# Kernel tuning notes

Hardware: AMD Instinct MI355X
Metric: run time of the kernel (lower is better)

Reference implementation:

```python
import jax, jax.numpy as jnp
import numpy as np

EMB = 256  # embedding_dim


def setup_inputs() -> dict:
    key = jax.random.key(0)
    ks = jax.random.split(key, 9)
    B, S, D = 4, 4096, EMB
    inputs = jax.random.normal(ks[0], (B, S, 3 * D), dtype=jnp.float32)
    def dense(kw, kb, d_in, d_out):
        w = jax.random.normal(kw, (d_in, d_out), dtype=jnp.float32) / np.sqrt(d_in)
        b = jnp.zeros((d_out,), dtype=jnp.float32)
        return w, b
    wq, bq = dense(ks[1], ks[2], D, D)
    wk, bk = dense(ks[3], ks[4], D, D)
    wv, bv = dense(ks[5], ks[6], D, D)
    wo, bo = dense(ks[7], ks[8], D, D)
    return {"inputs": inputs, "wq": wq, "bq": bq, "wk": wk, "bk": bk,
            "wv": wv, "bv": bv, "wo": wo, "bo": bo}


def reference(inputs, wq, bq, wk, bk, wv, bv, wo, bo):
    # split last axis into q,k,v parts: [B,S,D] each
    q_in, k_in, v_in = jnp.split(inputs, 3, axis=-1)
    q = q_in @ wq + bq
    k = k_in @ wk + bk
    v = v_in @ wv + bv
    dk = jnp.asarray(k.shape[-1], dtype=jnp.float32)
    # unfused SDPA exactly as source: matmul -> scale -> softmax -> matmul
    logits = jnp.einsum('bsd,btd->bst', q, k) / jnp.sqrt(dk)  # [B,S,S]
    attn = jax.nn.softmax(logits, axis=-1)
    x = jnp.einsum('bst,btd->bsd', attn, v)
    return x @ wo + bo
```

## Files before the change

### kernel.cpp

```cpp
#include <hip/hip_runtime.h>

typedef _Float16 f16;
typedef _Float16 f16x4 __attribute__((ext_vector_type(4)));
typedef _Float16 f16x8 __attribute__((ext_vector_type(8)));
typedef float f32x4  __attribute__((ext_vector_type(4)));

#define MFMAH(a, b, c) __builtin_amdgcn_mfma_f32_16x16x32_f16(a, b, c, 0, 0, 0)

constexpr int D = 256;
constexpr int S = 4096;
constexpr int BATCH = 4;
constexpr int NROWS = BATCH * S;
constexpr float SCALE = 0.0625f;
constexpr size_t NE = (size_t)NROWS * D;

__device__ __forceinline__ void gll16(const void* g, void* l) {
  __builtin_amdgcn_global_load_lds(
      (const __attribute__((address_space(1))) unsigned int*)g,
      (__attribute__((address_space(3))) unsigned int*)l, 16, 0, 0);
}

__global__ __launch_bounds__(256)
void prep_wt_kernel(const float* __restrict__ wq, const float* __restrict__ wk,
                    const float* __restrict__ wv, const float* __restrict__ wo,
                    f16* __restrict__ Wt)
{
  const int m = blockIdx.y;
  const float* w = (m == 0) ? wq : (m == 1) ? wk : (m == 2) ? wv : wo;
  int id = blockIdx.x * 256 + threadIdx.x;
  int n = id >> 8, k = id & 255;
  Wt[((size_t)m << 16) + n * 256 + k] = (f16)w[k * 256 + n];
}

__global__ __launch_bounds__(256)
void qkv_mfma_kernel(const float* __restrict__ in, const f16* __restrict__ Wt,
                     const float* __restrict__ bq, const float* __restrict__ bk,
                     const float* __restrict__ bv,
                     f16* __restrict__ Qh, f16* __restrict__ Kf, f16* __restrict__ Vf)
{
  __shared__ __align__(16) char smem[32768];
  const int m = blockIdx.y;
  const int tid = threadIdx.x, lane = tid & 63, w = tid >> 6;
  const int l15 = lane & 15, quad = lane >> 4;
  const int row0 = blockIdx.x * 64 + w * 16;
  const f16* Wm = Wt + ((size_t)m << 16);
  const float* bias = (m == 0) ? bq : (m == 1) ? bk : bv;

  f16x8 af[8];
  {
    const float* arow = in + (size_t)(row0 + l15) * 768 + m * 256 + quad * 8;
#pragma unroll
    for (int kc = 0; kc < 8; ++kc) {
      float4 a0 = *(const float4*)(arow + kc * 32);
      float4 a1 = *(const float4*)(arow + kc * 32 + 4);
      f16x8 a;
      a[0] = (f16)a0.x; a[1] = (f16)a0.y; a[2] = (f16)a0.z; a[3] = (f16)a0.w;
      a[4] = (f16)a1.x; a[5] = (f16)a1.y; a[6] = (f16)a1.z; a[7] = (f16)a1.w;
      af[kc] = a;
    }
  }

  auto stageB = [&](int buf, int kc) {
    char* base = smem + buf * 16384;
#pragma unroll
    for (int i = 0; i < 4; ++i) {
      int ct = 4 * w + i;
      gll16(Wm + (ct * 16 + l15) * 256 + kc * 32 + quad * 8,
            base + ct * 1024 + lane * 16);
    }
  };

  f32x4 acc[16];
#pragma unroll
  for (int ct = 0; ct < 16; ++ct) acc[ct] = (f32x4){0.f, 0.f, 0.f, 0.f};

  stageB(0, 0);
  for (int kc = 0; kc < 8; ++kc) {
    __syncthreads();
    if (kc < 7) stageB((kc + 1) & 1, kc + 1);
    const char* Bb = smem + (kc & 1) * 16384;
#pragma unroll
    for (int ct = 0; ct < 16; ++ct) {
      f16x8 b = *(const f16x8*)(Bb + ct * 1024 + lane * 16);
      acc[ct] = MFMAH(af[kc], b, acc[ct]);
    }
  }
  __syncthreads();

  const int b_ = row0 >> 12;

  if (m == 0) {
    f16* ws = (f16*)(smem + w * 8192);
#pragma unroll
    for (int ct = 0; ct < 16; ++ct) {
      float bct = bias[ct * 16 + l15];
#pragma unroll
      for (int r = 0; r < 4; ++r)
        ws[(quad * 4 + r) * 256 + ct * 16 + l15] = (f16)((acc[ct][r] + bct) * SCALE);
    }
    f16* dst = Qh + (size_t)row0 * 256;
#pragma unroll
    for (int i = 0; i < 8; ++i)
      *(uint4*)(dst + lane * 8 + i * 512) = *(const uint4*)(ws + lane * 8 + i * 512);
  } else if (m == 1) {
    f16* ws = (f16*)(smem + w * 8192);
#pragma unroll
    for (int ct = 0; ct < 16; ++ct) {
      float bct = bias[ct * 16 + l15];
      int base = (ct >> 1) * 512 + ((ct & 1) * 2 + (l15 >> 3)) * 128 + (l15 & 7);
#pragma unroll
      for (int r = 0; r < 4; ++r)
        ws[base + (quad * 4 + r) * 8] = (f16)(acc[ct][r] + bct);
    }
    const int g = (row0 & 4095) >> 4;
    f16* dst = Kf + ((size_t)(b_ * 256 + g)) * 8 * 512;
#pragma unroll
    for (int i = 0; i < 8; ++i)
      *(uint4*)(dst + lane * 8 + i * 512) = *(const uint4*)(ws + lane * 8 + i * 512);
  } else {
    const int t = w & 1;
    f16* ws = (f16*)(smem + (w >> 1) * 16384);
#pragma unroll
    for (int ct = 0; ct < 16; ++ct) {
      float bct = bias[ct * 16 + l15];
      int base = ct * 512 + quad * 128 + l15 * 8 + t * 4;
#pragma unroll
      for (int r = 0; r < 4; ++r)
        ws[base + r] = (f16)(acc[ct][r] + bct);
    }
    __syncthreads();
    const int gv0 = ((blockIdx.x * 64) & 4095) >> 5;
    f16* dst = Vf + ((size_t)(b_ * 128 + gv0)) * 16 * 512;
    const f16* src = (const f16*)smem;
#pragma unroll
    for (int i = 0; i < 8; ++i)
      *(uint4*)(dst + tid * 8 + i * 2048) = *(const uint4*)(src + tid * 8 + i * 2048);
  }
}

__global__ __launch_bounds__(256, 2)
void attn6_kernel(const f16* __restrict__ Qh, const char* __restrict__ Kf,
                  const char* __restrict__ Vf,
                  f16* __restrict__ Pp, float* __restrict__ Mp, float* __restrict__ Lp)
{
  __shared__ __align__(16) char KVs[2][32768];

  const int tid = threadIdx.x, lane = tid & 63, w = tid >> 6;
  const int l15 = lane & 15, quad = lane >> 4;

  const int bx    = blockIdx.x;
  const int combo = bx & 15;
  const int b     = combo & 3;
  const int kz    = combo >> 2;
  const int qb    = bx >> 4;
  const int qrow0 = qb * 128 + w * 32;
  const int grow  = b * 4096 + qrow0;

  f16x8 qf[2][8];
#pragma unroll
  for (int sub = 0; sub < 2; ++sub) {
    const size_t qoff = (size_t)(grow + sub * 16 + l15) * 256 + quad * 8;
#pragma unroll
    for (int kc = 0; kc < 8; ++kc)
      qf[sub][kc] = *(const f16x8*)(Qh + qoff + kc * 32);
  }

  const char* kg[4];
  const char* vg[4];
#pragma unroll
  for (int i = 0; i < 4; ++i) {
    int f = 4 * w + i;
    kg[i] = Kf + (((size_t)(b * 256 + kz * 64 + (f >> 3))) * 8 + (f & 7)) * 1024
               + lane * 16;
    vg[i] = Vf + (((size_t)(b * 128 + kz * 32)) * 16 + f) * 1024 + lane * 16;
  }
  auto stage = [&](int buf) {
    char* base = &KVs[buf][0];
#pragma unroll
    for (int i = 0; i < 4; ++i) { gll16(kg[i], base + (4 * w + i) * 1024); kg[i] += 16384; }
#pragma unroll
    for (int i = 0; i < 4; ++i) { gll16(vg[i], base + 16384 + (4 * w + i) * 1024); vg[i] += 16384; }
  };

  f32x4 o0[16], o1[16];
#pragma unroll
  for (int ct = 0; ct < 16; ++ct) {
    o0[ct] = (f32x4){0.f, 0.f, 0.f, 0.f};
    o1[ct] = (f32x4){0.f, 0.f, 0.f, 0.f};
  }
  float m0 = -3.0e38f, m1 = -3.0e38f, l0 = 0.f, l1 = 0.f;

  stage(0);

  for (int it = 0; it < 32; ++it) {
    __syncthreads();
    if (it < 31) stage((it + 1) & 1);
    const char* Bf = &KVs[it & 1][0];

    f32x4 sA0 = (f32x4){0.f,0.f,0.f,0.f}, sB0 = (f32x4){0.f,0.f,0.f,0.f};
    f32x4 sA1 = (f32x4){0.f,0.f,0.f,0.f}, sB1 = (f32x4){0.f,0.f,0.f,0.f};
#pragma unroll
    for (int kc = 0; kc < 8; ++kc) {
      f16x8 kA = *(const f16x8*)(Bf + kc * 1024 + lane * 16);
      f16x8 kB = *(const f16x8*)(Bf + 8192 + kc * 1024 + lane * 16);
      sA0 = MFMAH(kA, qf[0][kc], sA0);
      sA1 = MFMAH(kA, qf[1][kc], sA1);
      sB0 = MFMAH(kB, qf[0][kc], sB0);
      sB1 = MFMAH(kB, qf[1][kc], sB1);
    }

    float mn0, mn1, al0, al1;
    f16x8 ph0, ph1;
    {
      float t = fmaxf(fmaxf(fmaxf(sA0[0], sA0[1]), fmaxf(sA0[2], sA0[3])),
                      fmaxf(fmaxf(sB0[0], sB0[1]), fmaxf(sB0[2], sB0[3])));
      t = fmaxf(t, __shfl_xor(t, 16));
      t = fmaxf(t, __shfl_xor(t, 32));
      mn0 = fmaxf(m0, t);
      al0 = __expf(m0 - mn0);
      float ps = 0.f;
#pragma unroll
      for (int r = 0; r < 4; ++r) {
        float pa = __expf(sA0[r] - mn0);
        float pb = __expf(sB0[r] - mn0);
        ph0[r] = (f16)pa;  ph0[r + 4] = (f16)pb;
        ps += pa + pb;
      }
      ps += __shfl_xor(ps, 16);
      ps += __shfl_xor(ps, 32);
      l0 = l0 * al0 + ps;
    }
    {
      float t = fmaxf(fmaxf(fmaxf(sA1[0], sA1[1]), fmaxf(sA1[2], sA1[3])),
                      fmaxf(fmaxf(sB1[0], sB1[1]), fmaxf(sB1[2], sB1[3])));
      t = fmaxf(t, __shfl_xor(t, 16));
      t = fmaxf(t, __shfl_xor(t, 32));
      mn1 = fmaxf(m1, t);
      al1 = __expf(m1 - mn1);
      float ps = 0.f;
#pragma unroll
      for (int r = 0; r < 4; ++r) {
        float pa = __expf(sA1[r] - mn1);
        float pb = __expf(sB1[r] - mn1);
        ph1[r] = (f16)pa;  ph1[r + 4] = (f16)pb;
        ps += pa + pb;
      }
      ps += __shfl_xor(ps, 16);
      ps += __shfl_xor(ps, 32);
      l1 = l1 * al1 + ps;
    }

    if (__any(mn0 > m0)) {
      float a0 = __shfl(al0, (quad << 2) + 0);
      float a1 = __shfl(al0, (quad << 2) + 1);
      float a2 = __shfl(al0, (quad << 2) + 2);
      float a3 = __shfl(al0, (quad << 2) + 3);
#pragma unroll
      for (int ct = 0; ct < 16; ++ct) {
        o0[ct][0] *= a0; o0[ct][1] *= a1; o0[ct][2] *= a2; o0[ct][3] *= a3;
      }
    }
    if (__any(mn1 > m1)) {
      float a0 = __shfl(al1, (quad << 2) + 0);
      float a1 = __shfl(al1, (quad << 2) + 1);
      float a2 = __shfl(al1, (quad << 2) + 2);
      float a3 = __shfl(al1, (quad << 2) + 3);
#pragma unroll
      for (int ct = 0; ct < 16; ++ct) {
        o1[ct][0] *= a0; o1[ct][1] *= a1; o1[ct][2] *= a2; o1[ct][3] *= a3;
      }
    }
    m0 = mn0;  m1 = mn1;

#pragma unroll
    for (int ct = 0; ct < 16; ++ct) {
      f16x8 vf = *(const f16x8*)(Bf + 16384 + ct * 1024 + lane * 16);
      o0[ct] = MFMAH(ph0, vf, o0[ct]);
      o1[ct] = MFMAH(ph1, vf, o1[ct]);
    }
  }

  f16* Od = Pp + (size_t)kz * NE;
#pragma unroll
  for (int r = 0; r < 4; ++r) {
    const size_t ro0 = (size_t)(grow + quad * 4 + r) * 256 + l15;
    const size_t ro1 = (size_t)(grow + 16 + quad * 4 + r) * 256 + l15;
#pragma unroll
    for (int ct = 0; ct < 16; ++ct) {
      Od[ro0 + ct * 16] = (f16)o0[ct][r];
      Od[ro1 + ct * 16] = (f16)o1[ct][r];
    }
  }
  if (lane < 16) {
    Mp[kz * NROWS + grow + l15] = m0;
    Lp[kz * NROWS + grow + l15] = l0;
    Mp[kz * NROWS + grow + 16 + l15] = m1;
    Lp[kz * NROWS + grow + 16 + l15] = l1;
  }
}

__global__ __launch_bounds__(256)
void oproj_mfma_kernel(const f16* __restrict__ Pp, const float* __restrict__ Mp,
                       const float* __restrict__ Lp, const f16* __restrict__ Wto,
                       const float* __restrict__ bo, float* __restrict__ out)
{
  __shared__ f16 xs[32][264];
  __shared__ __align__(16) char Bs[2][16384];
  const int tid = threadIdx.x, lane = tid & 63, w = tid >> 6;
  const int l15 = lane & 15, quad = lane >> 4;
  const int rb = blockIdx.x * 32;

  auto stageB = [&](int buf, int kc) {
    char* base = &Bs[buf][0];
#pragma unroll
    for (int i = 0; i < 4; ++i) {
      int ct = 4 * w + i;
      gll16(Wto + (ct * 16 + l15) * 256 + kc * 32 + quad * 8,
            base + ct * 1024 + lane * 16);
    }
  };
  stageB(0, 0);

  const int c4 = (tid & 63) * 4;
  const int rsub = tid >> 6;
#pragma unroll
  for (int e = 0; e < 8; ++e) {
    int rl = e * 4 + rsub;
    int row = rb + rl;
    float m[4], l[4];
#pragma unroll
    for (int z = 0; z < 4; ++z) {
      m[z] = Mp[z * NROWS + row];
      l[z] = Lp[z * NROWS + row];
    }
    float mm = fmaxf(fmaxf(m[0], m[1]), fmaxf(m[2], m[3]));
    float wz[4], denom = 0.f;
#pragma unroll
    for (int z = 0; z < 4; ++z) { wz[z] = __expf(m[z] - mm); denom += wz[z] * l[z]; }
    float inv = 1.0f / denom;
    float s0 = 0.f, s1 = 0.f, s2 = 0.f, s3 = 0.f;
#pragma unroll
    for (int z = 0; z < 4; ++z) {
      f16x4 h = *(const f16x4*)(Pp + (size_t)z * NE + (size_t)row * 256 + c4);
      s0 += wz[z] * (float)h[0];
      s1 += wz[z] * (float)h[1];
      s2 += wz[z] * (float)h[2];
      s3 += wz[z] * (float)h[3];
    }
    f16x4 xv;
    xv[0] = (f16)(s0 * inv); xv[1] = (f16)(s1 * inv);
    xv[2] = (f16)(s2 * inv); xv[3] = (f16)(s3 * inv);
    *(f16x4*)&xs[rl][c4] = xv;
  }

  const int rw = (w & 1) * 16;
  const int cg = (w >> 1) * 8;
  f32x4 acc[8];
#pragma unroll
  for (int c = 0; c < 8; ++c) acc[c] = (f32x4){0.f, 0.f, 0.f, 0.f};

  for (int kc = 0; kc < 8; ++kc) {
    __syncthreads();
    if (kc < 7) stageB((kc + 1) & 1, kc + 1);
    const char* Bb = &Bs[kc & 1][0];
    f16x8 a = *(const f16x8*)&xs[rw + l15][kc * 32 + quad * 8];
#pragma unroll
    for (int c = 0; c < 8; ++c) {
      f16x8 b = *(const f16x8*)(Bb + (cg + c) * 1024 + lane * 16);
      acc[c] = MFMAH(a, b, acc[c]);
    }
  }

#pragma unroll
  for (int c = 0; c < 8; ++c) {
    int col = (cg + c) * 16 + l15;
    float bct = bo[col];
#pragma unroll
    for (int r = 0; r < 4; ++r)
      out[(size_t)(rb + rw + quad * 4 + r) * 256 + col] = acc[c][r] + bct;
  }
}

extern "C" void kernel_launch(void* const* d_in, const int* in_sizes, int n_in,
                              void* d_out, int out_size, void* d_ws, size_t ws_size,
                              hipStream_t stream)
{
  const float* inp = (const float*)d_in[0];
  const float* wq  = (const float*)d_in[1];
  const float* bq  = (const float*)d_in[2];
  const float* wk  = (const float*)d_in[3];
  const float* bk  = (const float*)d_in[4];
  const float* wv  = (const float*)d_in[5];
  const float* bv  = (const float*)d_in[6];
  const float* wo  = (const float*)d_in[7];
  const float* bo  = (const float*)d_in[8];
  float* out = (float*)d_out;

  f16* Qh = (f16*)d_ws;
  f16* Kf = Qh + NE;
  f16* Vf = Kf + NE;
  f16* Wt = Vf + NE;
  f16* Pp = Wt + 4 * 65536;
  float* Mp = (float*)(Pp + 4 * NE);
  float* Lp = Mp + 4 * NROWS;

  prep_wt_kernel<<<dim3(256, 4), 256, 0, stream>>>(wq, wk, wv, wo, Wt);

  qkv_mfma_kernel<<<dim3(256, 3), 256, 0, stream>>>(
      inp, Wt, bq, bk, bv, Qh, Kf, Vf);

  attn6_kernel<<<512, 256, 0, stream>>>(Qh, (const char*)Kf, (const char*)Vf,
                                        Pp, Mp, Lp);

  oproj_mfma_kernel<<<512, 256, 0, stream>>>(Pp, Mp, Lp, Wt + 3 * 65536, bo, out);
}
```

Measured before the change: 244.0 us.

## Shrink attention tiles to 16 keys per step with 2-wave blocks

The attention kernel now uses 128-thread blocks covering 64 query rows and processes 16 keys per iteration instead of 32. The PV product switches to the 16x16x16 MFMA, and the QKV projection writes V in a matching per-16-row fragment layout. Smaller blocks and half the LDS per block are meant to raise occupancy and give 1024 blocks for better load balance. The cost is twice as many loop iterations and barriers, and the K/V tiles in LDS are reused by fewer waves.

```diff
diff --git a/kernel.cpp b/kernel.cpp
--- a/kernel.cpp
+++ b/kernel.cpp
@@ -5,7 +5,8 @@
 typedef _Float16 f16x8 __attribute__((ext_vector_type(8)));
 typedef float f32x4  __attribute__((ext_vector_type(4)));
 
-#define MFMAH(a, b, c) __builtin_amdgcn_mfma_f32_16x16x32_f16(a, b, c, 0, 0, 0)
+#define MFMAH(a, b, c)   __builtin_amdgcn_mfma_f32_16x16x32_f16(a, b, c, 0, 0, 0)
+#define MFMAH16(a, b, c) __builtin_amdgcn_mfma_f32_16x16x16f16(a, b, c, 0, 0, 0)
 
 constexpr int D = 256;
 constexpr int S = 4096;
@@ -113,37 +114,35 @@
         ws[base + (quad * 4 + r) * 8] = (f16)(acc[ct][r] + bct);
     }
     const int g = (row0 & 4095) >> 4;
-    f16* dst = Kf + ((size_t)(b_ * 256 + g)) * 8 * 512;
+    f16* dst = Kf + ((size_t)(b_ * 256 + g)) * 4096;
 #pragma unroll
     for (int i = 0; i < 8; ++i)
       *(uint4*)(dst + lane * 8 + i * 512) = *(const uint4*)(ws + lane * 8 + i * 512);
   } else {
-    const int t = w & 1;
-    f16* ws = (f16*)(smem + (w >> 1) * 16384);
+    f16* ws = (f16*)(smem + w * 8192);
 #pragma unroll
     for (int ct = 0; ct < 16; ++ct) {
       float bct = bias[ct * 16 + l15];
-      int base = ct * 512 + quad * 128 + l15 * 8 + t * 4;
-#pragma unroll
-      for (int r = 0; r < 4; ++r)
-        ws[base + r] = (f16)(acc[ct][r] + bct);
-    }
-    __syncthreads();
-    const int gv0 = ((blockIdx.x * 64) & 4095) >> 5;
-    f16* dst = Vf + ((size_t)(b_ * 128 + gv0)) * 16 * 512;
-    const f16* src = (const f16*)smem;
+      int idx = (ct >> 1) * 512 + (ct & 1) * 256 + quad * 64 + l15 * 4;
+      f16x4 hv;
+#pragma unroll
+      for (int r = 0; r < 4; ++r) hv[r] = (f16)(acc[ct][r] + bct);
+      *(f16x4*)&ws[idx] = hv;
+    }
+    const int gv = (row0 & 4095) >> 4;
+    f16* dst = Vf + (size_t)(b_ * 256 + gv) * 4096;
 #pragma unroll
     for (int i = 0; i < 8; ++i)
-      *(uint4*)(dst + tid * 8 + i * 2048) = *(const uint4*)(src + tid * 8 + i * 2048);
-  }
-}
-
-__global__ __launch_bounds__(256, 2)
-void attn6_kernel(const f16* __restrict__ Qh, const char* __restrict__ Kf,
+      *(uint4*)(dst + lane * 8 + i * 512) = *(const uint4*)(ws + lane * 8 + i * 512);
+  }
+}
+
+__global__ __launch_bounds__(128, 3)
+void attn9_kernel(const f16* __restrict__ Qh, const char* __restrict__ Kf,
                   const char* __restrict__ Vf,
                   f16* __restrict__ Pp, float* __restrict__ Mp, float* __restrict__ Lp)
 {
-  __shared__ __align__(16) char KVs[2][32768];
+  __shared__ __align__(16) char KVs[2][16384];
 
   const int tid = threadIdx.x, lane = tid & 63, w = tid >> 6;
   const int l15 = lane & 15, quad = lane >> 4;
@@ -153,7 +152,7 @@
   const int b     = combo & 3;
   const int kz    = combo >> 2;
   const int qb    = bx >> 4;
-  const int qrow0 = qb * 128 + w * 32;
+  const int qrow0 = qb * 64 + w * 32;
   const int grow  = b * 4096 + qrow0;
 
   f16x8 qf[2][8];
@@ -170,16 +169,15 @@
 #pragma unroll
   for (int i = 0; i < 4; ++i) {
     int f = 4 * w + i;
-    kg[i] = Kf + (((size_t)(b * 256 + kz * 64 + (f >> 3))) * 8 + (f & 7)) * 1024
-               + lane * 16;
-    vg[i] = Vf + (((size_t)(b * 128 + kz * 32)) * 16 + f) * 1024 + lane * 16;
+    kg[i] = Kf + (((size_t)(b * 256 + kz * 64)) * 8 + f) * 1024 + lane * 16;
+    vg[i] = Vf + (((size_t)(b * 256 + kz * 64)) * 8 + f) * 1024 + lane * 16;
   }
   auto stage = [&](int buf) {
     char* base = &KVs[buf][0];
 #pragma unroll
-    for (int i = 0; i < 4; ++i) { gll16(kg[i], base + (4 * w + i) * 1024); kg[i] += 16384; }
-#pragma unroll
-    for (int i = 0; i < 4; ++i) { gll16(vg[i], base + 16384 + (4 * w + i) * 1024); vg[i] += 16384; }
+    for (int i = 0; i < 4; ++i) { gll16(kg[i], base + (4 * w + i) * 1024); kg[i] += 8192; }
+#pragma unroll
+    for (int i = 0; i < 4; ++i) { gll16(vg[i], base + 8192 + (4 * w + i) * 1024); vg[i] += 8192; }
   };
 
   f32x4 o0[16], o1[16];
@@ -192,62 +190,49 @@
 
   stage(0);
 
-  for (int it = 0; it < 32; ++it) {
+  for (int it = 0; it < 64; ++it) {
     __syncthreads();
-    if (it < 31) stage((it + 1) & 1);
+    if (it < 63) stage((it + 1) & 1);
     const char* Bf = &KVs[it & 1][0];
 
-    f32x4 sA0 = (f32x4){0.f,0.f,0.f,0.f}, sB0 = (f32x4){0.f,0.f,0.f,0.f};
-    f32x4 sA1 = (f32x4){0.f,0.f,0.f,0.f}, sB1 = (f32x4){0.f,0.f,0.f,0.f};
+    f32x4 s0 = (f32x4){0.f,0.f,0.f,0.f};
+    f32x4 s1 = (f32x4){0.f,0.f,0.f,0.f};
 #pragma unroll
     for (int kc = 0; kc < 8; ++kc) {
       f16x8 kA = *(const f16x8*)(Bf + kc * 1024 + lane * 16);
-      f16x8 kB = *(const f16x8*)(Bf + 8192 + kc * 1024 + lane * 16);
-      sA0 = MFMAH(kA, qf[0][kc], sA0);
-      sA1 = MFMAH(kA, qf[1][kc], sA1);
-      sB0 = MFMAH(kB, qf[0][kc], sB0);
-      sB1 = MFMAH(kB, qf[1][kc], sB1);
+      s0 = MFMAH(kA, qf[0][kc], s0);
+      s1 = MFMAH(kA, qf[1][kc], s1);
     }
 
     float mn0, mn1, al0, al1;
-    f16x8 ph0, ph1;
+    f16x4 pah0, pah1;
     {
-      float t = fmaxf(fmaxf(fmaxf(sA0[0], sA0[1]), fmaxf(sA0[2], sA0[3])),
-                      fmaxf(fmaxf(sB0[0], sB0[1]), fmaxf(sB0[2], sB0[3])));
+      float t = fmaxf(fmaxf(s0[0], s0[1]), fmaxf(s0[2], s0[3]));
       t = fmaxf(t, __shfl_xor(t, 16));
       t = fmaxf(t, __shfl_xor(t, 32));
       mn0 = fmaxf(m0, t);
       al0 = __expf(m0 - mn0);
-      float ps = 0.f;
-#pragma unroll
-      for (int r = 0; r < 4; ++r) {
-        float pa = __expf(sA0[r] - mn0);
-        float pb = __expf(sB0[r] - mn0);
-        ph0[r] = (f16)pa;  ph0[r + 4] = (f16)pb;
-        ps += pa + pb;
-      }
+      float p0 = __expf(s0[0] - mn0), p1 = __expf(s0[1] - mn0);
+      float p2 = __expf(s0[2] - mn0), p3 = __expf(s0[3] - mn0);
+      float ps = (p0 + p1) + (p2 + p3);
       ps += __shfl_xor(ps, 16);
       ps += __shfl_xor(ps, 32);
       l0 = l0 * al0 + ps;
+      pah0[0] = (f16)p0; pah0[1] = (f16)p1; pah0[2] = (f16)p2; pah0[3] = (f16)p3;
     }
     {
-      float t = fmaxf(fmaxf(fmaxf(sA1[0], sA1[1]), fmaxf(sA1[2], sA1[3])),
-                      fmaxf(fmaxf(sB1[0], sB1[1]), fmaxf(sB1[2], sB1[3])));
+      float t = fmaxf(fmaxf(s1[0], s1[1]), fmaxf(s1[2], s1[3]));
       t = fmaxf(t, __shfl_xor(t, 16));
       t = fmaxf(t, __shfl_xor(t, 32));
       mn1 = fmaxf(m1, t);
       al1 = __expf(m1 - mn1);
-      float ps = 0.f;
-#pragma unroll
-      for (int r = 0; r < 4; ++r) {
-        float pa = __expf(sA1[r] - mn1);
-        float pb = __expf(sB1[r] - mn1);
-        ph1[r] = (f16)pa;  ph1[r + 4] = (f16)pb;
-        ps += pa + pb;
-      }
+      float p0 = __expf(s1[0] - mn1), p1 = __expf(s1[1] - mn1);
+      float p2 = __expf(s1[2] - mn1), p3 = __expf(s1[3] - mn1);
+      float ps = (p0 + p1) + (p2 + p3);
       ps += __shfl_xor(ps, 16);
       ps += __shfl_xor(ps, 32);
       l1 = l1 * al1 + ps;
+      pah1[0] = (f16)p0; pah1[1] = (f16)p1; pah1[2] = (f16)p2; pah1[3] = (f16)p3;
     }
 
     if (__any(mn0 > m0)) {
@@ -274,9 +259,9 @@
 
 #pragma unroll
     for (int ct = 0; ct < 16; ++ct) {
-      f16x8 vf = *(const f16x8*)(Bf + 16384 + ct * 1024 + lane * 16);
-      o0[ct] = MFMAH(ph0, vf, o0[ct]);
-      o1[ct] = MFMAH(ph1, vf, o1[ct]);
+      f16x4 vf4 = *(const f16x4*)(Bf + 8192 + ct * 512 + lane * 8);
+      o0[ct] = MFMAH16(pah0, vf4, o0[ct]);
+      o1[ct] = MFMAH16(pah1, vf4, o1[ct]);
     }
   }
 
@@ -409,8 +394,8 @@
   qkv_mfma_kernel<<<dim3(256, 3), 256, 0, stream>>>(
       inp, Wt, bq, bk, bv, Qh, Kf, Vf);
 
-  attn6_kernel<<<512, 256, 0, stream>>>(Qh, (const char*)Kf, (const char*)Vf,
-                                        Pp, Mp, Lp);
+  attn9_kernel<<<1024, 128, 0, stream>>>(Qh, (const char*)Kf, (const char*)Vf,
+                                         Pp, Mp, Lp);
 
   oproj_mfma_kernel<<<512, 256, 0, stream>>>(Pp, Mp, Lp, Wt + 3 * 65536, bo, out);
 }
```

Result: slower. 519.8 us (+113.0%).
